# Optimization experiments

Hardware: AMD Instinct MI355X
Metric: run time of the kernel (lower is better)

The kernel has to match this reference:

```python
import jax, jax.numpy as jnp
import numpy as np

B, L, NC, D = 4, 2048, 4096, 128
ITERS = 4
NHEAD = 8
T = L // 2
C2 = 2 * D


def _ln(x, g, b, eps=1e-5):
    m = jnp.mean(x, axis=-1, keepdims=True)
    v = jnp.var(x, axis=-1, keepdims=True)
    return (x - m) * jax.lax.rsqrt(v + eps) * g + b


def _mlp3(x, W1, b1, W2, b2, W3, b3):
    h = jax.nn.relu(x @ W1 + b1)
    h = jax.nn.relu(h @ W2 + b2)
    return h @ W3 + b3


def _lstm(inp, h, c, Wih, Whh, gi, bi, gh, bh, gc, bc):
    gates = _ln(inp @ Wih, gi, bi) + _ln(h @ Whh, gh, bh)
    i, f, g, o = jnp.split(gates, 4, axis=-1)
    cy = _ln(jax.nn.sigmoid(f) * c + jax.nn.sigmoid(i) * jnp.tanh(g), gc, bc)
    hy = jax.nn.sigmoid(o) * jnp.tanh(cy)
    return hy, cy


def _flip(x):
    # flip matrix with full literal counts == permutation swapping pos/neg halves
    half = x.shape[1] // 2
    return jnp.concatenate([x[:, half:], x[:, :half]], axis=1)


def setup_inputs():
    key = jax.random.key(0)
    ks = iter(jax.random.split(key, 64))
    def xav(fi, fo):
        s = float(np.sqrt(6.0 / (fi + fo)))
        return jax.random.uniform(next(ks), (fi, fo), jnp.float32, -s, s)
    def rn(*shape):
        return jax.random.normal(next(ks), shape, jnp.float32)
    inp = {}
    inp['adjacency_matrices'] = (jax.random.uniform(next(ks), (B, L, NC)) < 0.03).astype(jnp.float32)
    inp['batch_lit_counts'] = jnp.full((B,), L, dtype=jnp.int32)
    inp['L_init'] = rn(1, D) / np.sqrt(D).astype(np.float32)
    inp['C_init'] = rn(1, D) / np.sqrt(D).astype(np.float32)
    for p in ('LC', 'CL'):
        for i in (1, 2, 3):
            inp[p + '_W' + str(i)] = xav(D, D)
            inp[p + '_b' + str(i)] = jnp.full((D,), 0.01, jnp.float32)
    for p, isz in (('Lu', 2 * D), ('Cu', D)):
        inp[p + '_Wih'] = rn(isz, 4 * D)  # torch uses raw randn for LSTM weights
        inp[p + '_Whh'] = rn(D, 4 * D)
        for ln, n in (('lni', 4 * D), ('lnh', 4 * D), ('lnc', D)):
            inp[p + '_' + ln + '_g'] = jnp.ones((n,), jnp.float32)
            inp[p + '_' + ln + '_b'] = jnp.zeros((n,), jnp.float32)
    for p in ('k', 'q', 'v'):
        inp['att_W' + p] = xav(C2, C2)
        inp['att_b' + p] = jnp.zeros((C2,), jnp.float32)
    for p in ('asn', 'vote'):
        inp[p + '_W1'] = xav(C2, D)
        inp[p + '_b1'] = jnp.full((D,), 0.01, jnp.float32)
        inp[p + '_W2'] = xav(D, 1)
        inp[p + '_b2'] = jnp.full((1,), 0.01, jnp.float32)
    return inp


def reference(adjacency_matrices, batch_lit_counts, L_init, C_init,
              LC_W1, LC_b1, LC_W2, LC_b2, LC_W3, LC_b3,
              CL_W1, CL_b1, CL_W2, CL_b2, CL_W3, CL_b3,
              Lu_Wih, Lu_Whh, Lu_lni_g, Lu_lni_b, Lu_lnh_g, Lu_lnh_b, Lu_lnc_g, Lu_lnc_b,
              Cu_Wih, Cu_Whh, Cu_lni_g, Cu_lni_b, Cu_lnh_g, Cu_lnh_b, Cu_lnc_g, Cu_lnc_b,
              att_Wk, att_bk, att_Wq, att_bq, att_Wv, att_bv,
              asn_W1, asn_b1, asn_W2, asn_b2, vote_W1, vote_b1, vote_W2, vote_b2):
    A = adjacency_matrices
    Bb, Ll, Cc = A.shape
    Lh = jnp.broadcast_to(L_init, (Bb, Ll, D))
    Lc = jnp.zeros_like(Lh)
    Ch = jnp.broadcast_to(C_init, (Bb, Cc, D))
    Cxc = jnp.zeros_like(Ch)
    for _ in range(ITERS):
        # literal -> clause messages (gather via A^T)
        LC = jnp.einsum('blc,bld->bcd', A, _mlp3(Lh, LC_W1, LC_b1, LC_W2, LC_b2, LC_W3, LC_b3))
        Ch, Cxc = _lstm(LC, Ch, Cxc, Cu_Wih, Cu_Whh, Cu_lni_g, Cu_lni_b, Cu_lnh_g, Cu_lnh_b, Cu_lnc_g, Cu_lnc_b)
        # clause -> literal messages (scatter via A)
        CL = jnp.einsum('blc,bcd->bld', A, _mlp3(Ch, CL_W1, CL_b1, CL_W2, CL_b2, CL_W3, CL_b3))
        Lh, Lc = _lstm(jnp.concatenate([CL, _flip(Lh)], axis=-1), Lh, Lc,
                       Lu_Wih, Lu_Whh, Lu_lni_g, Lu_lni_b, Lu_lnh_g, Lu_lnh_b, Lu_lnc_g, Lu_lnc_b)
    # readout [h_l ; h_{~l}], positive literals only
    read = jnp.concatenate([Lh, _flip(Lh)], axis=-1)[:, :T]  # [B,T,2D]
    half = batch_lit_counts // 2
    mask = (jnp.arange(T)[None, :] < half[:, None]).astype(read.dtype)  # [B,T]
    read = read * mask[:, :, None]
    hd = C2 // NHEAD
    def heads(x, W, b):
        return (x @ W + b).reshape(Bb, T, NHEAD, hd).transpose(0, 2, 1, 3)
    k = heads(read, att_Wk, att_bk)
    q = heads(read, att_Wq, att_bq)
    v = heads(read, att_Wv, att_bv)
    att = jnp.einsum('bhtd,bhsd->bhts', q, k) * (1.0 / np.sqrt(hd))
    sq = (mask[:, None, :, None] * mask[:, None, None, :]) > 0  # [B,1,T,T]
    att = jnp.where(sq, att, -jnp.inf)
    att = jax.nn.softmax(att, axis=-1)
    att = jnp.where(jnp.isnan(att), 0.0, att)
    y = jnp.einsum('bhts,bhsd->bhtd', att, v).transpose(0, 2, 1, 3).reshape(Bb, T, C2)
    def head_mlp(x, W1, b1, W2, b2):
        return jax.nn.sigmoid(jax.nn.relu(x @ W1 + b1) @ W2 + b2)[..., 0]
    assignments = head_mlp(y, asn_W1, asn_b1, asn_W2, asn_b2) * mask  # [B,T]
    vote_vals = head_mlp(y, vote_W1, vote_b1, vote_W2, vote_b2)
    votes = jnp.sum(vote_vals * mask, axis=1) / jnp.maximum(jnp.sum(mask, axis=1), 1.0)
    return votes, assignments
```

## Files before the change

kernel.cpp:

```cpp
#include <hip/hip_runtime.h>


#define B_    4
#define L_    2048
#define NC_   4096
#define D_    128
#define ITERS_ 4
#define NH_   8
#define T_    1024
#define C2_   256
#define HD_   32
#define BL_   (B_*L_)
#define BNC_  (B_*NC_)
#define QS_   768

typedef unsigned short u16;
typedef __attribute__((ext_vector_type(8))) short b16x8;
typedef __attribute__((ext_vector_type(4))) float f32x4;

static __device__ __forceinline__ float bf2f(u16 u){
  union{unsigned int i; float f;} x; x.i = ((unsigned int)u) << 16; return x.f;
}
static __device__ __forceinline__ u16 f2bf(float f){
  union{float f; unsigned int i;} x; x.f = f;
// ... 111 lines not shown
  if ((w & 63) == 0) ss[w >> 6] = pc;
  __syncthreads();
  if (w == 0) cnt_l[row] = ss[0] + ss[1];
}

__global__ __launch_bounds__(256) void k_scan(unsigned* __restrict__ cnt,
    unsigned* __restrict__ off, int n){
  __shared__ unsigned ps[257];
  int t = threadIdx.x;
  int seg = n >> 8;
  int base = t*seg;
  unsigned s = 0;
  for (int i = 0; i < seg; i++) s += cnt[base+i];
  ps[t] = s;
  __syncthreads();
  if (t == 0){
    unsigned run = 0;
    for (int i = 0; i < 256; i++){ unsigned x = ps[i]; ps[i] = run; run += x; }
    ps[256] = run;
  }
  __syncthreads();
  unsigned run = ps[t];
  for (int i = 0; i < seg; i++){ off[base+i] = run; run += cnt[base+i]; cnt[base+i] = 0u; }
  if (t == 0) off[n] = ps[256];
}

__global__ __launch_bounds__(128) void k_fill_l(const unsigned* __restrict__ bits,
    const unsigned* __restrict__ off_l, u16* __restrict__ val_l,
    unsigned* __restrict__ cnt_c){
  const int row = blockIdx.x, w = threadIdx.x;
  const int b = row >> 11;
  unsigned m = bits[(size_t)row*128 + w];
  unsigned pc = __popc(m);
  __shared__ unsigned s[128];
  s[w] = pc; __syncthreads();
  #pragma unroll
  for (int o = 1; o < 128; o <<= 1){
    unsigned v = (w >= o) ? s[w-o] : 0u;
    __syncthreads();
    s[w] += v;
    __syncthreads();
  }
  unsigned base = off_l[row] + s[w] - pc;
  unsigned cb = ((unsigned)b << 12) + w*32;
  while (m){
    int j = __ffs(m) - 1; m &= m - 1;
    val_l[base++] = (u16)(w*32 + j);
    atomicAdd(cnt_c + cb + j, 1u);
  }
}

__global__ __launch_bounds__(256) void k_fill_c(const unsigned* __restrict__ bits,
    const unsigned* __restrict__ off_c, unsigned* __restrict__ cur_c,
    u16* __restrict__ val_c){
  int g = blockIdx.x*256 + threadIdx.x;
  unsigned m = bits[g];
  int row = g >> 7, w = g & 127;
  int b = row >> 11, l = row & (L_-1);
  unsigned cb = ((unsigned)b << 12) + w*32;
  while (m){
    int j = __ffs(m) - 1; m &= m - 1;
    unsigned idx = cb + j;
    unsigned pos = atomicAdd(cur_c + idx, 1u);
    val_c[off_c[idx] + pos] = (u16)l;
  }
}

__global__ __launch_bounds__(256) void k_spmm(const unsigned* __restrict__ off,
    const u16* __restrict__ val, const float* __restrict__ M, float* __restrict__ out,
    int sh1, int sh2){
  int row  = blockIdx.x*4 + (threadIdx.x >> 6);
  int lane = threadIdx.x & 63;
  unsigned p0 = off[row], p1 = off[row+1];
  const float2* Mp = (const float2*)M + (((size_t)(row >> sh1) << sh2) * 64) + lane;
  float x = 0.f, y = 0.f;
  for (unsigned p = p0; p < p1; ++p){
    float2 v = Mp[(size_t)val[p] * 64];
    x += v.x; y += v.y;
  }
  float2 r; r.x = x; r.y = y;
  ((float2*)out)[(size_t)row*64 + lane] = r;
}

__global__ __launch_bounds__(256) void k_mlp3m(const float* __restrict__ X,
    const u16* __restrict__ W1h, const u16* __restrict__ W1l,
    const u16* __restrict__ W2h, const u16* __restrict__ W2l,
    const u16* __restrict__ W3h, const u16* __restrict__ W3l,
    const float* __restrict__ b1, const float* __restrict__ b2,
    const float* __restrict__ b3, float* __restrict__ Y)
{
  __shared__ __align__(16) u16 Ah[32*136];
  __shared__ __align__(16) u16 Al[32*136];
  const int tid = threadIdx.x, lane = tid & 63, wv = tid >> 6;
  const int quad = lane >> 4, l15 = lane & 15;
  const int r0 = blockIdx.x * 32;
  {
    int row = tid >> 3, c0 = (tid & 7)*16;
    const float4* src = (const float4*)(X + (size_t)(r0+row)*128 + c0);
    #pragma unroll
    for (int q4 = 0; q4 < 4; q4++){
      float4 v = src[q4]; int k = c0 + q4*4;
      u16 h,l;
      split2(v.x,h,l); Ah[row*136+k]  =h; Al[row*136+k]  =l;
      split2(v.y,h,l); Ah[row*136+k+1]=h; Al[row*136+k+1]=l;
      split2(v.z,h,l); Ah[row*136+k+2]=h; Al[row*136+k+2]=l;
      split2(v.w,h,l); Ah[row*136+k+3]=h; Al[row*136+k+3]=l;
    }
  }
  __syncthreads();
  const u16* Whs[3] = {W1h, W2h, W3h};
  const u16* Wls[3] = {W1l, W2l, W3l};
  const float* bs[3] = {b1, b2, b3};
  #pragma unroll
  for (int layer = 0; layer < 3; layer++){
    f32x4 acc[2][2] = {};
    #pragma unroll
    for (int ks = 0; ks < 4; ks++){
      b16x8 a_h[2], a_l[2];
      #pragma unroll
      for (int mt = 0; mt < 2; mt++){
        int ao = (mt*16 + l15)*136 + ks*32 + quad*8;
        a_h[mt] = *(const b16x8*)(Ah + ao);
        a_l[mt] = *(const b16x8*)(Al + ao);
      }
      #pragma unroll
      for (int ntl = 0; ntl < 2; ntl++){
        int nt = wv*2 + ntl;
        size_t bo = (size_t)((nt*4 + ks)*64 + lane)*8;
        b16x8 bh = *(const b16x8*)(Whs[layer] + bo);
        b16x8 bl = *(const b16x8*)(Wls[layer] + bo);
        #pragma unroll
        for (int mt = 0; mt < 2; mt++){
          acc[mt][ntl] = __builtin_amdgcn_mfma_f32_16x16x32_bf16(a_h[mt], bh, acc[mt][ntl],0,0,0);
          acc[mt][ntl] = __builtin_amdgcn_mfma_f32_16x16x32_bf16(a_h[mt], bl, acc[mt][ntl],0,0,0);
          acc[mt][ntl] = __builtin_amdgcn_mfma_f32_16x16x32_bf16(a_l[mt], bh, acc[mt][ntl],0,0,0);
        }
      }
    }
    if (layer < 2){
      __syncthreads();
      #pragma unroll
      for (int mt = 0; mt < 2; mt++)
        #pragma unroll
        for (int ntl = 0; ntl < 2; ntl++){
          int col = wv*32 + ntl*16 + l15;
          float bb = bs[layer][col];
          #pragma unroll
          for (int r = 0; r < 4; r++){
            int row = mt*16 + quad*4 + r;
            float v = fmaxf(acc[mt][ntl][r] + bb, 0.f);
            u16 h,l; split2(v,h,l);
            Ah[row*136 + col] = h; Al[row*136 + col] = l;
          }
        }
      __syncthreads();
    } else {
      #pragma unroll
      for (int mt = 0; mt < 2; mt++)
        #pragma unroll
        for (int ntl = 0; ntl < 2; ntl++){
          int col = wv*32 + ntl*16 + l15;
          float bb = bs[2][col];
          #pragma unroll
          for (int r = 0; r < 4; r++){
            int row = mt*16 + quad*4 + r;
            Y[(size_t)(r0+row)*128 + col] = acc[mt][ntl][r] + bb;
          }
        }
    }
  }
}

template<int NSEG>
__global__ __launch_bounds__(256) void k_lstm_mfma(
    const float* __restrict__ A0, const float* __restrict__ A1, const float* __restrict__ A2,
    int flip1,
    const u16* __restrict__ W0h, const u16* __restrict__ W0l,
    const u16* __restrict__ W1h, const u16* __restrict__ W1l,
    const u16* __restrict__ W2h, const u16* __restrict__ W2l,
    const float* __restrict__ lni_g, const float* __restrict__ lni_b,
    const float* __restrict__ lnh_g, const float* __restrict__ lnh_b,
    const float* __restrict__ lnc_g, const float* __restrict__ lnc_b,
    const float* __restrict__ c_in, float* __restrict__ c_out,
    float* __restrict__ h_out)
{
  __shared__ __align__(16) float G[32*516];
  __shared__ float red[4][32][4];
  __shared__ float st[32][4];
  u16* Ah = (u16*)G;
  u16* Al = Ah + 32*136;
  const int tid = threadIdx.x, lane = tid & 63, wv = tid >> 6;
  const int quad = lane >> 4, l15 = lane & 15;
  const int r0 = blockIdx.x * 32;

  f32x4 acc1[2][8] = {}, acc2[2][8] = {};

  #pragma unroll
  for (int s = 0; s < NSEG; ++s){
    const float* Ap = (s==0) ? A0 : ((s==1) ? A1 : A2);
    const u16* Wh = (s==0) ? W0h : ((s==1) ? W1h : W2h);
    const u16* Wl = (s==0) ? W0l : ((s==1) ? W1l : W2l);
    const int fm = (s==1) ? flip1 : 0;
    __syncthreads();
    {
      int row = tid >> 3, c0 = (tid & 7)*16;
      int arow = (r0 + row) ^ fm;
      const float4* src = (const float4*)(Ap + (size_t)arow*128 + c0);
      #pragma unroll
      for (int q4 = 0; q4 < 4; q4++){
        float4 v = src[q4]; int k = c0 + q4*4;
        u16 h,l;
        split2(v.x,h,l); Ah[row*136+k]  =h; Al[row*136+k]  =l;
        split2(v.y,h,l); Ah[row*136+k+1]=h; Al[row*136+k+1]=l;
        split2(v.z,h,l); Ah[row*136+k+2]=h; Al[row*136+k+2]=l;
        split2(v.w,h,l); Ah[row*136+k+3]=h; Al[row*136+k+3]=l;
      }
    }
    __syncthreads();
    f32x4 (*accp)[8] = (s == NSEG-1) ? acc2 : acc1;
    #pragma unroll
    for (int ks = 0; ks < 4; ks++){
      b16x8 a_h[2], a_l[2];
      #pragma unroll
      for (int mt = 0; mt < 2; mt++){
        int ao = (mt*16 + l15)*136 + ks*32 + quad*8;
        a_h[mt] = *(const b16x8*)(Ah + ao);
        a_l[mt] = *(const b16x8*)(Al + ao);
      }
      #pragma unroll
      for (int ntl = 0; ntl < 8; ntl++){
        int nt = wv*8 + ntl;
        size_t bo = (size_t)((nt*4 + ks)*64 + lane)*8;
        b16x8 bh = *(const b16x8*)(Wh + bo);
        b16x8 bl = *(const b16x8*)(Wl + bo);
        #pragma unroll
        for (int mt = 0; mt < 2; mt++){
          accp[mt][ntl] = __builtin_amdgcn_mfma_f32_16x16x32_bf16(a_h[mt], bh, accp[mt][ntl],0,0,0);
          accp[mt][ntl] = __builtin_amdgcn_mfma_f32_16x16x32_bf16(a_h[mt], bl, accp[mt][ntl],0,0,0);
          accp[mt][ntl] = __builtin_amdgcn_mfma_f32_16x16x32_bf16(a_l[mt], bh, accp[mt][ntl],0,0,0);
        }
      }
    }
  }

  #pragma unroll
  for (int mt = 0; mt < 2; mt++)
    #pragma unroll
    for (int r = 0; r < 4; r++){
      float s1=0.f, q1=0.f, s2=0.f, q2=0.f;
      #pragma unroll
      for (int ntl = 0; ntl < 8; ntl++){
        float v1 = acc1[mt][ntl][r]; s1 += v1; q1 += v1*v1;
        float v2 = acc2[mt][ntl][r]; s2 += v2; q2 += v2*v2;
      }
      #pragma unroll
      for (int m = 1; m < 16; m <<= 1){
        s1 += __shfl_xor(s1, m); q1 += __shfl_xor(q1, m);
        s2 += __shfl_xor(s2, m); q2 += __shfl_xor(q2, m);
      }
      if (l15 == 0){
        int row = mt*16 + quad*4 + r;
        red[wv][row][0]=s1; red[wv][row][1]=q1; red[wv][row][2]=s2; red[wv][row][3]=q2;
      }
    }
  __syncthreads();
  if (tid < 32){
    int row = tid;
    float s1 = red[0][row][0]+red[1][row][0]+red[2][row][0]+red[3][row][0];
    float q1 = red[0][row][1]+red[1][row][1]+red[2][row][1]+red[3][row][1];
    float s2 = red[0][row][2]+red[1][row][2]+red[2][row][2]+red[3][row][2];
    float q2 = red[0][row][3]+red[1][row][3]+red[2][row][3]+red[3][row][3];
    const float i512 = 1.f/512.f;
    float m1 = s1*i512, v1 = fmaxf(q1*i512 - m1*m1, 0.f);
    float m2 = s2*i512, v2 = fmaxf(q2*i512 - m2*m2, 0.f);
    st[row][0] = m1; st[row][1] = rsqrtf(v1 + 1e-5f);
    st[row][2] = m2; st[row][3] = rsqrtf(v2 + 1e-5f);
  }
  __syncthreads();

  #pragma unroll
  for (int mt = 0; mt < 2; mt++)
    #pragma unroll
    for (int ntl = 0; ntl < 8; ntl++){
      int col = wv*128 + ntl*16 + l15;
      float gi = lni_g[col], bi = lni_b[col];
      float gh = lnh_g[col], bh = lnh_b[col];
      #pragma unroll
      for (int r = 0; r < 4; r++){
        int row = mt*16 + quad*4 + r;
        float v = (acc1[mt][ntl][r] - st[row][0])*st[row][1]*gi + bi
                + (acc2[mt][ntl][r] - st[row][2])*st[row][3]*gh + bh;
        G[row*516 + col] = v;
      }
    }
  __syncthreads();

  float lcg0 = lnc_g[lane], lcb0 = lnc_b[lane];
  float lcg1 = lnc_g[lane+64], lcb1 = lnc_b[lane+64];
  const float i128 = 1.f/128.f;
  #pragma unroll
  for (int i = 0; i < 8; i++){
    int row = wv*8 + i;
    int rg = r0 + row;
    float cp[2], sc = 0.f, qc = 0.f;
    #pragma unroll
    for (int jj = 0; jj < 2; jj++){
      int c = lane + 64*jj;
      float iv = sigm(G[row*516 + c]);
      float fv = sigm(G[row*516 + 128 + c]);
      float gv = tanhf(G[row*516 + 256 + c]);
      cp[jj] = fv * c_in[(size_t)rg*128 + c] + iv*gv;
      sc += cp[jj]; qc += cp[jj]*cp[jj];
    }
    #pragma unroll
    for (int m = 1; m < 64; m <<= 1){ sc += __shfl_xor(sc, m); qc += __shfl_xor(qc, m); }
    float mc = sc*i128, vc = fmaxf(qc*i128 - mc*mc, 0.f), rsc = rsqrtf(vc + 1e-5f);
    #pragma unroll
    for (int jj = 0; jj < 2; jj++){
      int c = lane + 64*jj;
      float cy = (cp[jj]-mc)*rsc*(jj ? lcg1 : lcg0) + (jj ? lcb1 : lcb0);
      c_out[(size_t)rg*128 + c] = cy;
      float ov = sigm(G[row*516 + 384 + c]);
      h_out[(size_t)rg*128 + c] = ov*tanhf(cy);
    }
  }
}

template<int NT, int KK32, int ACT>
__global__ __launch_bounds__(256) void k_gemm_mfma(const float* __restrict__ A,
    const u16* __restrict__ Wh, const u16* __restrict__ Wl,
    const float* __restrict__ bias, float* __restrict__ Y)
{
  const int N = NT*64;
  const int LDA = KK32*32 + 8;
  __shared__ __align__(16) u16 Ah[32*(KK32*32+8)];
  __shared__ __align__(16) u16 Al[32*(KK32*32+8)];
  const int tid = threadIdx.x, lane = tid & 63, wv = tid >> 6;
  const int quad = lane >> 4, l15 = lane & 15;
  const int r0 = blockIdx.x * 32;
  {
    int row = tid >> 3, c0 = (tid & 7)*(KK32*4);
    const float4* src = (const float4*)(A + (size_t)(r0+row)*(KK32*32) + c0);
    #pragma unroll
    for (int q4 = 0; q4 < KK32; q4++){
      float4 v = src[q4]; int k = c0 + q4*4;
      u16 h,l;
      split2(v.x,h,l); Ah[row*LDA+k]  =h; Al[row*LDA+k]  =l;
      split2(v.y,h,l); Ah[row*LDA+k+1]=h; Al[row*LDA+k+1]=l;
      split2(v.z,h,l); Ah[row*LDA+k+2]=h; Al[row*LDA+k+2]=l;
      split2(v.w,h,l); Ah[row*LDA+k+3]=h; Al[row*LDA+k+3]=l;
    }
  }
  __syncthreads();
  f32x4 acc[2][NT] = {};
  #pragma unroll
  for (int ks = 0; ks < KK32; ks++){
    b16x8 a_h[2], a_l[2];
    #pragma unroll
    for (int mt = 0; mt < 2; mt++){
      int ao = (mt*16 + l15)*LDA + ks*32 + quad*8;
      a_h[mt] = *(const b16x8*)(Ah + ao);
      a_l[mt] = *(const b16x8*)(Al + ao);
    }
    #pragma unroll
    for (int ntl = 0; ntl < NT; ntl++){
      int nt = wv*NT + ntl;
      size_t bo = (size_t)((nt*KK32 + ks)*64 + lane)*8;
      b16x8 bh = *(const b16x8*)(Wh + bo);
      b16x8 bl = *(const b16x8*)(Wl + bo);
      #pragma unroll
      for (int mt = 0; mt < 2; mt++){
        acc[mt][ntl] = __builtin_amdgcn_mfma_f32_16x16x32_bf16(a_h[mt], bh, acc[mt][ntl],0,0,0);
        acc[mt][ntl] = __builtin_amdgcn_mfma_f32_16x16x32_bf16(a_h[mt], bl, acc[mt][ntl],0,0,0);
        acc[mt][ntl] = __builtin_amdgcn_mfma_f32_16x16x32_bf16(a_l[mt], bh, acc[mt][ntl],0,0,0);
      }
    }
  }
  #pragma unroll
  for (int mt = 0; mt < 2; mt++)
    #pragma unroll
    for (int ntl = 0; ntl < NT; ntl++){
      int col = wv*(NT*16) + ntl*16 + l15;
      float bb = bias[col];
      #pragma unroll
      for (int r = 0; r < 4; r++){
        int row = mt*16 + quad*4 + r;
        float v = acc[mt][ntl][r] + bb;
        if (ACT) v = fmaxf(v, 0.f);
        Y[(size_t)(r0+row)*N + col] = v;
      }
    }
}

__global__ __launch_bounds__(256) void k_read(const float* __restrict__ Lh,
    const int* __restrict__ counts, float* __restrict__ rd)
{
  int i = blockIdx.x*256 + threadIdx.x;
  if (i >= B_*T_*D_) return;
  int d = i & (D_-1);
  int r = i >> 7;
  int t = r & (T_-1);
  int b = r >> 10;
  int half = counts[b] / 2; if (half > T_) half = T_;
  float m = (t < half) ? 1.f : 0.f;
  rd[(size_t)r*C2_ + d]      = m * Lh[(size_t)(b*L_ + t)*D_ + d];
  rd[(size_t)r*C2_ + D_ + d] = m * Lh[(size_t)(b*L_ + t + T_)*D_ + d];
}

__global__ __launch_bounds__(256) void k_attn_tile(const float* __restrict__ qkv,
    const int* __restrict__ counts, float* __restrict__ y)
{
  const int b = blockIdx.z, h = blockIdx.y, t0 = blockIdx.x*64;
  int half = counts[b] / 2; if (half > T_) half = T_; if (half < 0) half = 0;
  const int tid = threadIdx.x;
  const int lane = tid & 63, wv = tid >> 6;
  const int lr = tid >> 2, lc = (tid & 3)*8;

  if (t0 >= half){
    float* yp = y + ((size_t)(b*T_ + t0 + lr)*C2_ + h*HD_ + lc);
    #pragma unroll
    for (int j = 0; j < 8; j++) yp[j] = 0.f;
    return;
  }

  __shared__ float Qs[64][36];
  __shared__ float Ks[64][32];
  __shared__ float Ss[64][68];

  {
    const float* qp = qkv + (size_t)(b*T_ + t0 + lr)*QS_ + h*HD_ + lc;
    float4 a0 = *(const float4*)qp;
    float4 a1 = *(const float4*)(qp+4);
    *(float4*)&Qs[lr][lc]   = a0;
    *(float4*)&Qs[lr][lc+4] = a1;
  }

  const int ty = tid >> 4, tx = tid & 15;
  const int sr = wv*16 + (lane & 15);
  const int spart = (lane >> 4) * 16;
  const int rp = lane >> 3, cq = lane & 7;
  const int r0 = wv*16 + rp*2;

  float4 acc0 = {0.f,0.f,0.f,0.f}, acc1 = {0.f,0.f,0.f,0.f};
  float mst = -3e38f, lst = 0.f;
  const float scale = 0.17677669529663687f;
  const int nt = (half + 63) >> 6;

  for (int st = 0; st < nt; ++st){
    const int s0 = st*64;
    __syncthreads();
    {
      const float* kp = qkv + (size_t)(b*T_ + s0 + lr)*QS_ + 256 + h*HD_ + lc;
      float4 k0 = *(const float4*)kp;
      float4 k1 = *(const float4*)(kp+4);
      int key = (lr >> 2) & 7;
      int c0 = lc >> 2;
      *(float4*)&Ks[lr][4*((c0  ) ^ key)] = k0;
      *(float4*)&Ks[lr][4*((c0+1) ^ key)] = k1;
    }
    __syncthreads();

    float s4[4][4];
    #pragma unroll
    for (int i = 0; i < 4; i++)
      #pragma unroll
      for (int j = 0; j < 4; j++) s4[i][j] = 0.f;
    const int xk = tx & 7;
    #pragma unroll
    for (int kk4 = 0; kk4 < 8; kk4++){
      float4 a4[4], b4[4];
      #pragma unroll
      for (int i = 0; i < 4; i++) a4[i] = *(const float4*)&Qs[ty*4+i][kk4*4];
      const int pk = 4*(kk4 ^ xk);
      #pragma unroll
      for (int j = 0; j < 4; j++) b4[j] = *(const float4*)&Ks[tx*4+j][pk];
      #pragma unroll
      for (int i = 0; i < 4; i++)
        #pragma unroll
        for (int j = 0; j < 4; j++)
          s4[i][j] += a4[i].x*b4[j].x + a4[i].y*b4[j].y + a4[i].z*b4[j].z + a4[i].w*b4[j].w;
    }
    #pragma unroll
    for (int i = 0; i < 4; i++){
      float4 w4;
      w4.x = (s0 + tx*4 + 0 < half) ? s4[i][0]*scale : -1e30f;
      w4.y = (s0 + tx*4 + 1 < half) ? s4[i][1]*scale : -1e30f;
      w4.z = (s0 + tx*4 + 2 < half) ? s4[i][2]*scale : -1e30f;
      w4.w = (s0 + tx*4 + 3 < half) ? s4[i][3]*scale : -1e30f;
      *(float4*)&Ss[ty*4+i][tx*4] = w4;
    }

    float pvv[16];
    float vmax = -3e38f;
    #pragma unroll
    for (int c4 = 0; c4 < 4; c4++){
      float4 t4 = *(const float4*)&Ss[sr][spart + c4*4];
      pvv[c4*4+0] = t4.x; pvv[c4*4+1] = t4.y; pvv[c4*4+2] = t4.z; pvv[c4*4+3] = t4.w;
      vmax = fmaxf(vmax, fmaxf(fmaxf(t4.x, t4.y), fmaxf(t4.z, t4.w)));
    }
    vmax = fmaxf(vmax, __shfl_xor(vmax, 16));
    vmax = fmaxf(vmax, __shfl_xor(vmax, 32));
    float nm = fmaxf(mst, vmax);
    float alpha = expf(mst - nm);
    float psum = 0.f;
    #pragma unroll
    for (int c = 0; c < 16; c++){
      float p = expf(pvv[c] - nm);
      pvv[c] = p; psum += p;
    }
    psum += __shfl_xor(psum, 16);
    psum += __shfl_xor(psum, 32);
    lst = lst*alpha + psum;
    mst = nm;
    #pragma unroll
    for (int c4 = 0; c4 < 4; c4++){
      float4 w4; w4.x = pvv[c4*4+0]; w4.y = pvv[c4*4+1]; w4.z = pvv[c4*4+2]; w4.w = pvv[c4*4+3];
      *(float4*)&Ss[sr][spart + c4*4] = w4;
    }
    float al0 = __shfl(alpha, 2*rp);
    float al1 = __shfl(alpha, 2*rp + 1);
    acc0.x *= al0; acc0.y *= al0; acc0.z *= al0; acc0.w *= al0;
    acc1.x *= al1; acc1.y *= al1; acc1.z *= al1; acc1.w *= al1;

    const float* vbase = qkv + (size_t)(b*T_ + s0)*QS_ + 512 + h*HD_ + cq*4;
    #pragma unroll 4
    for (int kk4 = 0; kk4 < 16; kk4++){
      float4 p0 = *(const float4*)&Ss[r0  ][kk4*4];
      float4 p1 = *(const float4*)&Ss[r0+1][kk4*4];
      float4 v0 = *(const float4*)(vbase + (size_t)(kk4*4+0)*QS_);
      float4 v1 = *(const float4*)(vbase + (size_t)(kk4*4+1)*QS_);
      float4 v2 = *(const float4*)(vbase + (size_t)(kk4*4+2)*QS_);
      float4 v3 = *(const float4*)(vbase + (size_t)(kk4*4+3)*QS_);
      acc0.x += p0.x*v0.x + p0.y*v1.x + p0.z*v2.x + p0.w*v3.x;
      acc0.y += p0.x*v0.y + p0.y*v1.y + p0.z*v2.y + p0.w*v3.y;
      acc0.z += p0.x*v0.z + p0.y*v1.z + p0.z*v2.z + p0.w*v3.z;
      acc0.w += p0.x*v0.w + p0.y*v1.w + p0.z*v2.w + p0.w*v3.w;
      acc1.x += p1.x*v0.x + p1.y*v1.x + p1.z*v2.x + p1.w*v3.x;
      acc1.y += p1.x*v0.y + p1.y*v1.y + p1.z*v2.y + p1.w*v3.y;
      acc1.z += p1.x*v0.z + p1.y*v1.z + p1.z*v2.z + p1.w*v3.z;
      acc1.w += p1.x*v0.w + p1.y*v1.w + p1.z*v2.w + p1.w*v3.w;
    }
  }

  float l0 = __shfl(lst, 2*rp);
  float l1 = __shfl(lst, 2*rp + 1);
  float m0 = (t0 + r0     < half && l0 > 0.f) ? 1.f/l0 : 0.f;
  float m1 = (t0 + r0 + 1 < half && l1 > 0.f) ? 1.f/l1 : 0.f;
  float4 o0, o1;
  o0.x = acc0.x*m0; o0.y = acc0.y*m0; o0.z = acc0.z*m0; o0.w = acc0.w*m0;
  o1.x = acc1.x*m1; o1.y = acc1.y*m1; o1.z = acc1.z*m1; o1.w = acc1.w*m1;
  *(float4*)(y + ((size_t)(b*T_ + t0 + r0    )*C2_ + h*HD_ + cq*4)) = o0;
  *(float4*)(y + ((size_t)(b*T_ + t0 + r0 + 1)*C2_ + h*HD_ + cq*4)) = o1;
}

__global__ __launch_bounds__(128) void k_final(const float* __restrict__ hv,
    const float* __restrict__ aW2, const float* __restrict__ ab2,
    const float* __restrict__ vW2, const float* __restrict__ vb2,
    const int* __restrict__ counts, void* __restrict__ outv,
    float* __restrict__ vote_sum, const int* __restrict__ flag)
{
  int row = blockIdx.x, tid = threadIdx.x;
  int b = row / T_, t = row - b*T_;
  int half = counts[b] / 2; if (half > T_) half = T_;
  float pa = hv[(size_t)row*256 + tid]       * aW2[tid];
  float pv = hv[(size_t)row*256 + 128 + tid] * vW2[tid];
  #pragma unroll
  for (int off = 32; off > 0; off >>= 1){ pa += __shfl_down(pa, off); pv += __shfl_down(pv, off); }
  __shared__ float r[2][2];
  int wid = tid >> 6, lane = tid & 63;
  if (lane == 0){ r[0][wid] = pa; r[1][wid] = pv; }
  __syncthreads();
  if (tid == 0){
    float a  = sigm(r[0][0] + r[0][1] + ab2[0]);
    float vv = sigm(r[1][0] + r[1][1] + vb2[0]);
    bool mk = (t < half);
    float av = mk ? a : 0.f;
    if (*flag) ((u16*)outv)[4 + row] = f2bf(av);
    else       ((float*)outv)[4 + row] = av;
    if (mk) atomicAdd(vote_sum + b, vv);
  }
}

__global__ void k_votes(const float* __restrict__ vote_sum, const int* __restrict__ counts,
                        void* __restrict__ outv, const int* __restrict__ flag){
  int b = threadIdx.x;
  if (b < B_){
    int half = counts[b] / 2; if (half > T_) half = T_;
    float den = (float)(half > 1 ? half : 1);
    float vv = vote_sum[b] / den;
    if (*flag) ((u16*)outv)[b] = f2bf(vv);
    else       ((float*)outv)[b] = vv;
  }
}

extern "C" void kernel_launch(void* const* d_in, const int* in_sizes, int n_in,
                              void* d_out, int out_size, void* d_ws, size_t ws_size,
                              hipStream_t stream)
{
  const void* A_adj = d_in[0];
  const int* counts = (const int*)d_in[1];

  const size_t M1 = (size_t)1048576;
  const size_t NEED = (5*M1 + M1 + 2*M1 + 2*M1 + 700416 + 16416 + 8224
                       + 16384 + 8192 + 520000 + 520000 + 32) * sizeof(float);
  if (ws_size < NEED) return;

  float* ws = (float*)d_ws;
  float* R    = ws;
  float* Lc   = R + 5*M1;
  float* Ch   = Lc + M1;
  float* Cc   = Ch + 2*M1;
  float* wp   = Cc + 2*M1;
  unsigned* off_c = (unsigned*)(wp + 700416);
  unsigned* off_l = off_c + 16416;
  unsigned* cnt_c = off_l + 8224;
  unsigned* cnt_l = cnt_c + 16384;
  u16* val_c = (u16*)(cnt_l + 8192);
  u16* val_l = (u16*)((float*)val_c + 520000);
  float* tail = (float*)val_l + 520000;
  float* vote_sum = tail;
  int* flag = (int*)(tail + 8);
  unsigned* bits = (unsigned*)R;

  float* R0 = R, *R1 = R + M1, *R2 = R + 2*M1, *R3 = R + 3*M1, *R4 = R + 4*M1;

  k_detect<<<1, 256, 0, stream>>>((const unsigned int*)A_adj, flag);

  CJobs cj;
  int ncj = 0;
  unsigned off = 0;
  auto cadd = [&](int idx, unsigned n)->float*{
    cj.src[ncj] = d_in[idx]; cj.n[ncj] = n; cj.off[ncj] = off;
    float* p = wp + off; off += (n + 3u) & ~3u; ncj++; return p;
  };
  float* Linit = cadd(2, 128);
  float* Cinit = cadd(3, 128);
  float *LC_b1 = cadd(5, 128), *LC_b2 = cadd(7, 128), *LC_b3 = cadd(9, 128);
  float *CL_b1 = cadd(11,128), *CL_b2 = cadd(13,128), *CL_b3 = cadd(15,128);
  float *Lu_lni_g = cadd(18,512), *Lu_lni_b = cadd(19,512);
  float *Lu_lnh_g = cadd(20,512), *Lu_lnh_b = cadd(21,512);
  float *Lu_lnc_g = cadd(22,128), *Lu_lnc_b = cadd(23,128);
  float *Cu_lni_g = cadd(26,512), *Cu_lni_b = cadd(27,512);
  float *Cu_lnh_g = cadd(28,512), *Cu_lnh_b = cadd(29,512);
  float *Cu_lnc_g = cadd(30,128), *Cu_lnc_b = cadd(31,128);
  float *asn_W2 = cadd(40,128), *asn_b2 = cadd(41,1);
  float *vote_W2 = cadd(44,128), *vote_b2 = cadd(45,1);
  float* bqkv = wp + off;
  cj.src[ncj]=d_in[35]; cj.n[ncj]=256; cj.off[ncj]=off;       ncj++;
  cj.src[ncj]=d_in[33]; cj.n[ncj]=256; cj.off[ncj]=off+256;   ncj++;
  cj.src[ncj]=d_in[37]; cj.n[ncj]=256; cj.off[ncj]=off+512;   ncj++;
  off += 768;
  float* bhv = wp + off;
  cj.src[ncj]=d_in[39]; cj.n[ncj]=128; cj.off[ncj]=off;       ncj++;
  cj.src[ncj]=d_in[43]; cj.n[ncj]=128; cj.off[ncj]=off+128;   ncj++;
  off += 256;
  { dim3 g(2, NCJ_); k_cvt_all<<<g, 256, 0, stream>>>(cj, wp, flag); }

  u16* up = (u16*)(wp + ((off + 3u) & ~3u));
  PJobs pj;
  int npj = 0;
  unsigned uoff = 0;
  auto padd = [&](int idx, unsigned n, unsigned Nw, unsigned koff, unsigned ksb,
                  unsigned dsth, unsigned dstl){
    pj.src[npj]=d_in[idx]; pj.n[npj]=n; pj.N[npj]=Nw; pj.koff[npj]=koff;
    pj.ksb[npj]=ksb; pj.dh[npj]=dsth; pj.dl[npj]=dstl; npj++;
  };
  auto solo = [&](int idx, unsigned n, unsigned Nw, unsigned koff, unsigned ksb,
                  const u16** h, const u16** l){
    padd(idx, n, Nw, koff, ksb, uoff, uoff + n);
    *h = up + uoff; *l = up + uoff + n; uoff += 2*n;
  };
  const u16 *lc1h,*lc1l,*lc2h,*lc2l,*lc3h,*lc3l,*cl1h,*cl1l,*cl2h,*cl2l,*cl3h,*cl3l;
  const u16 *cwih_h,*cwih_l,*cwhh_h,*cwhh_l;
  const u16 *lwa_h,*lwa_l,*lwb_h,*lwb_l,*lwhh_h,*lwhh_l;
  solo(4, 16384,128,0,2,&lc1h,&lc1l);  solo(6, 16384,128,0,2,&lc2h,&lc2l);
  solo(8, 16384,128,0,2,&lc3h,&lc3l);  solo(10,16384,128,0,2,&cl1h,&cl1l);
  solo(12,16384,128,0,2,&cl2h,&cl2l);  solo(14,16384,128,0,2,&cl3h,&cl3l);
  solo(24,65536,512,0,2,&cwih_h,&cwih_l);
  solo(25,65536,512,0,2,&cwhh_h,&cwhh_l);
  solo(16,65536,512,0,  2,&lwa_h,&lwa_l);
  solo(16,65536,512,128,2,&lwb_h,&lwb_l);
  solo(17,65536,512,0,2,&lwhh_h,&lwhh_l);
  const u16* wqkv_h = up + uoff;
  const u16* wqkv_l = up + uoff + 196608;
  padd(34, 65536, 256, 0, 3, uoff,           uoff+196608);
  padd(32, 65536, 256, 0, 3, uoff+65536,     uoff+196608+65536);
  padd(36, 65536, 256, 0, 3, uoff+131072,    uoff+196608+131072);
  uoff += 393216;
  const u16* whv_h = up + uoff;
  const u16* whv_l = up + uoff + 65536;
  padd(38, 32768, 128, 0, 3, uoff,        uoff+65536);
  padd(42, 32768, 128, 0, 3, uoff+32768,  uoff+65536+32768);
  uoff += 131072;
  { dim3 g(256, NPJ_); k_prep<<<g, 256, 0, stream>>>(pj, up, flag); }

  k_zero_u<<<(16384+255)/256, 256, 0, stream>>>(cnt_c, 16384);
  k_pack<<<BL_, 128, 0, stream>>>(A_adj, bits, cnt_l, flag);
  k_scan<<<1, 256, 0, stream>>>(cnt_l, off_l, 8192);
  k_fill_l<<<BL_, 128, 0, stream>>>(bits, off_l, val_l, cnt_c);
  k_scan<<<1, 256, 0, stream>>>(cnt_c, off_c, 16384);
  k_fill_c<<<4096, 256, 0, stream>>>(bits, off_c, cnt_c, val_c);

  k_init<<<(BL_*D_)/256, 256, 0, stream>>>(R0, Lc, Linit, BL_*D_);
  k_init<<<(BNC_*D_)/256, 256, 0, stream>>>(Ch, Cc, Cinit, BNC_*D_);

  for (int it = 0; it < ITERS_; ++it){
    bool ev = ((it & 1) == 0);
    float* cur  = ev ? R0 : R4;
    float* msgL = ev ? R1 : R0;
    float* LCb  = ev ? R2 : R1;
    float* msgC = LCb;
    float* CLb  = ev ? R1 : R3;
    float* nxt  = ev ? R4 : R0;

    k_mlp3m<<<BL_/32, 256, 0, stream>>>(cur, lc1h,lc1l, lc2h,lc2l, lc3h,lc3l,
                                        LC_b1, LC_b2, LC_b3, msgL);
    k_spmm<<<BNC_/4, 256, 0, stream>>>(off_c, val_c, msgL, LCb, 12, 11);
    k_lstm_mfma<2><<<BNC_/32, 256, 0, stream>>>(LCb, Ch, nullptr, 0,
        cwih_h, cwih_l, cwhh_h, cwhh_l, nullptr, nullptr,
        Cu_lni_g, Cu_lni_b, Cu_lnh_g, Cu_lnh_b, Cu_lnc_g, Cu_lnc_b, Cc, Cc, Ch);
    k_mlp3m<<<BNC_/32, 256, 0, stream>>>(Ch, cl1h,cl1l, cl2h,cl2l, cl3h,cl3l,
                                         CL_b1, CL_b2, CL_b3, msgC);
    k_spmm<<<BL_/4, 256, 0, stream>>>(off_l, val_l, msgC, CLb, 11, 12);
    k_lstm_mfma<3><<<BL_/32, 256, 0, stream>>>(CLb, cur, cur, 1024,
        lwa_h, lwa_l, lwb_h, lwb_l, lwhh_h, lwhh_l,
        Lu_lni_g, Lu_lni_b, Lu_lnh_g, Lu_lnh_b, Lu_lnc_g, Lu_lnc_b, Lc, Lc, nxt);
  }
  float* Lh = R0;

  float* readb = Lc;
  float* qkvb  = Ch;
  float* yb    = R1;
  float* hv    = R2;

  k_read<<<(B_*T_*D_)/256, 256, 0, stream>>>(Lh, counts, readb);
  k_gemm_mfma<12,8,0><<<(B_*T_)/32, 256, 0, stream>>>(readb, wqkv_h, wqkv_l, bqkv, qkvb);
  { dim3 g(T_/64, NH_, B_); k_attn_tile<<<g, 256, 0, stream>>>(qkvb, counts, yb); }
  k_gemm_mfma<4,8,1><<<(B_*T_)/32, 256, 0, stream>>>(yb, whv_h, whv_l, bhv, hv);
  k_zero<<<1, 64, 0, stream>>>(vote_sum, B_);
  k_final<<<B_*T_, 128, 0, stream>>>(hv, asn_W2, asn_b2, vote_W2, vote_b2,
                                     counts, d_out, vote_sum, flag);
  k_votes<<<1, 64, 0, stream>>>(vote_sum, counts, d_out, flag);
}
```

Measured before the change: 1.909 ms.

## Widen MFMA kernels to 512 threads, fuse read gather, split attention KV

The MLP, LSTM and dense GEMM kernels now run 8 waves per block, with fewer output tiles per wave, and the GEMMs also split columns over a second grid dimension. The separate read/mask kernel is folded into the QKV GEMM as a masked gather. Attention is split into two key halves computed in parallel, then merged by a new combine kernel using log-sum-exp weights. The aim is more parallelism and less register pressure per wave, at the cost of redundant A-tile staging per column split and an extra kernel launch plus partial-result traffic for attention.

```diff
diff --git a/kernel.cpp b/kernel.cpp
--- a/kernel.cpp
+++ b/kernel.cpp
@@ -217,7 +217,7 @@
   ((float2*)out)[(size_t)row*64 + lane] = r;
 }
 
-__global__ __launch_bounds__(256) void k_mlp3m(const float* __restrict__ X,
+__global__ __launch_bounds__(512) void k_mlp3m(const float* __restrict__ X,
     const u16* __restrict__ W1h, const u16* __restrict__ W1l,
     const u16* __restrict__ W2h, const u16* __restrict__ W2l,
     const u16* __restrict__ W3h, const u16* __restrict__ W3l,
@@ -230,17 +230,18 @@
   const int quad = lane >> 4, l15 = lane & 15;
   const int r0 = blockIdx.x * 32;
   {
-    int row = tid >> 3, c0 = (tid & 7)*16;
+    int row = tid >> 4, c0 = (tid & 15)*8;
     const float4* src = (const float4*)(X + (size_t)(r0+row)*128 + c0);
-    #pragma unroll
-    for (int q4 = 0; q4 < 4; q4++){
-      float4 v = src[q4]; int k = c0 + q4*4;
-      u16 h,l;
-      split2(v.x,h,l); Ah[row*136+k]  =h; Al[row*136+k]  =l;
-      split2(v.y,h,l); Ah[row*136+k+1]=h; Al[row*136+k+1]=l;
-      split2(v.z,h,l); Ah[row*136+k+2]=h; Al[row*136+k+2]=l;
-      split2(v.w,h,l); Ah[row*136+k+3]=h; Al[row*136+k+3]=l;
-    }
+    float4 v0 = src[0], v1 = src[1];
+    u16 h,l;
+    split2(v0.x,h,l); Ah[row*136+c0]  =h; Al[row*136+c0]  =l;
+    split2(v0.y,h,l); Ah[row*136+c0+1]=h; Al[row*136+c0+1]=l;
+    split2(v0.z,h,l); Ah[row*136+c0+2]=h; Al[row*136+c0+2]=l;
+    split2(v0.w,h,l); Ah[row*136+c0+3]=h; Al[row*136+c0+3]=l;
+    split2(v1.x,h,l); Ah[row*136+c0+4]=h; Al[row*136+c0+4]=l;
+    split2(v1.y,h,l); Ah[row*136+c0+5]=h; Al[row*136+c0+5]=l;
+    split2(v1.z,h,l); Ah[row*136+c0+6]=h; Al[row*136+c0+6]=l;
+    split2(v1.w,h,l); Ah[row*136+c0+7]=h; Al[row*136+c0+7]=l;
   }
   __syncthreads();
   const u16* Whs[3] = {W1h, W2h, W3h};
@@ -248,7 +249,7 @@
   const float* bs[3] = {b1, b2, b3};
   #pragma unroll
   for (int layer = 0; layer < 3; layer++){
-    f32x4 acc[2][2] = {};
+    f32x4 acc[2] = {};
     #pragma unroll
     for (int ks = 0; ks < 4; ks++){
       b16x8 a_h[2], a_l[2];
@@ -258,56 +259,45 @@
         a_h[mt] = *(const b16x8*)(Ah + ao);
         a_l[mt] = *(const b16x8*)(Al + ao);
       }
-      #pragma unroll
-      for (int ntl = 0; ntl < 2; ntl++){
-        int nt = wv*2 + ntl;
-        size_t bo = (size_t)((nt*4 + ks)*64 + lane)*8;
-        b16x8 bh = *(const b16x8*)(Whs[layer] + bo);
-        b16x8 bl = *(const b16x8*)(Wls[layer] + bo);
-        #pragma unroll
-        for (int mt = 0; mt < 2; mt++){
-          acc[mt][ntl] = __builtin_amdgcn_mfma_f32_16x16x32_bf16(a_h[mt], bh, acc[mt][ntl],0,0,0);
-          acc[mt][ntl] = __builtin_amdgcn_mfma_f32_16x16x32_bf16(a_h[mt], bl, acc[mt][ntl],0,0,0);
-          acc[mt][ntl] = __builtin_amdgcn_mfma_f32_16x16x32_bf16(a_l[mt], bh, acc[mt][ntl],0,0,0);
-        }
-      }
-    }
+      size_t bo = (size_t)((wv*4 + ks)*64 + lane)*8;
+      b16x8 bh = *(const b16x8*)(Whs[layer] + bo);
+      b16x8 bl = *(const b16x8*)(Wls[layer] + bo);
+      #pragma unroll
+      for (int mt = 0; mt < 2; mt++){
+        acc[mt] = __builtin_amdgcn_mfma_f32_16x16x32_bf16(a_h[mt], bh, acc[mt],0,0,0);
+        acc[mt] = __builtin_amdgcn_mfma_f32_16x16x32_bf16(a_h[mt], bl, acc[mt],0,0,0);
+        acc[mt] = __builtin_amdgcn_mfma_f32_16x16x32_bf16(a_l[mt], bh, acc[mt],0,0,0);
+      }
+    }
+    int col = wv*16 + l15;
     if (layer < 2){
+      float bb = bs[layer][col];
       __syncthreads();
       #pragma unroll
       for (int mt = 0; mt < 2; mt++)
         #pragma unroll
-        for (int ntl = 0; ntl < 2; ntl++){
-          int col = wv*32 + ntl*16 + l15;
-          float bb = bs[layer][col];
-          #pragma unroll
-          for (int r = 0; r < 4; r++){
-            int row = mt*16 + quad*4 + r;
-            float v = fmaxf(acc[mt][ntl][r] + bb, 0.f);
-            u16 h,l; split2(v,h,l);
-            Ah[row*136 + col] = h; Al[row*136 + col] = l;
-          }
+        for (int r = 0; r < 4; r++){
+          int row = mt*16 + quad*4 + r;
+          float v = fmaxf(acc[mt][r] + bb, 0.f);
+          u16 h,l; split2(v,h,l);
+          Ah[row*136 + col] = h; Al[row*136 + col] = l;
         }
       __syncthreads();
     } else {
+      float bb = bs[2][col];
       #pragma unroll
       for (int mt = 0; mt < 2; mt++)
         #pragma unroll
-        for (int ntl = 0; ntl < 2; ntl++){
-          int col = wv*32 + ntl*16 + l15;
-          float bb = bs[2][col];
-          #pragma unroll
-          for (int r = 0; r < 4; r++){
-            int row = mt*16 + quad*4 + r;
-            Y[(size_t)(r0+row)*128 + col] = acc[mt][ntl][r] + bb;
-          }
+        for (int r = 0; r < 4; r++){
+          int row = mt*16 + quad*4 + r;
+          Y[(size_t)(r0+row)*128 + col] = acc[mt][r] + bb;
         }
     }
   }
 }
 
 template<int NSEG>
-__global__ __launch_bounds__(256) void k_lstm_mfma(
+__global__ __launch_bounds__(512) void k_lstm_mfma(
     const float* __restrict__ A0, const float* __restrict__ A1, const float* __restrict__ A2,
     int flip1,
     const u16* __restrict__ W0h, const u16* __restrict__ W0l,
@@ -320,7 +310,7 @@
     float* __restrict__ h_out)
 {
   __shared__ __align__(16) float G[32*516];
-  __shared__ float red[4][32][4];
+  __shared__ float red[8][32][4];
   __shared__ float st[32][4];
   u16* Ah = (u16*)G;
   u16* Al = Ah + 32*136;
@@ -328,7 +318,7 @@
   const int quad = lane >> 4, l15 = lane & 15;
   const int r0 = blockIdx.x * 32;
 
-  f32x4 acc1[2][8] = {}, acc2[2][8] = {};
+  f32x4 acc1[2][4] = {}, acc2[2][4] = {};
 
   #pragma unroll
   for (int s = 0; s < NSEG; ++s){
@@ -338,21 +328,22 @@
     const int fm = (s==1) ? flip1 : 0;
     __syncthreads();
     {
-      int row = tid >> 3, c0 = (tid & 7)*16;
+      int row = tid >> 4, c0 = (tid & 15)*8;
       int arow = (r0 + row) ^ fm;
       const float4* src = (const float4*)(Ap + (size_t)arow*128 + c0);
-      #pragma unroll
-      for (int q4 = 0; q4 < 4; q4++){
-        float4 v = src[q4]; int k = c0 + q4*4;
-        u16 h,l;
-        split2(v.x,h,l); Ah[row*136+k]  =h; Al[row*136+k]  =l;
-        split2(v.y,h,l); Ah[row*136+k+1]=h; Al[row*136+k+1]=l;
-        split2(v.z,h,l); Ah[row*136+k+2]=h; Al[row*136+k+2]=l;
-        split2(v.w,h,l); Ah[row*136+k+3]=h; Al[row*136+k+3]=l;
-      }
+      float4 v0 = src[0], v1 = src[1];
+      u16 h,l;
+      split2(v0.x,h,l); Ah[row*136+c0]  =h; Al[row*136+c0]  =l;
+      split2(v0.y,h,l); Ah[row*136+c0+1]=h; Al[row*136+c0+1]=l;
+      split2(v0.z,h,l); Ah[row*136+c0+2]=h; Al[row*136+c0+2]=l;
+      split2(v0.w,h,l); Ah[row*136+c0+3]=h; Al[row*136+c0+3]=l;
+      split2(v1.x,h,l); Ah[row*136+c0+4]=h; Al[row*136+c0+4]=l;
+      split2(v1.y,h,l); Ah[row*136+c0+5]=h; Al[row*136+c0+5]=l;
+      split2(v1.z,h,l); Ah[row*136+c0+6]=h; Al[row*136+c0+6]=l;
+      split2(v1.w,h,l); Ah[row*136+c0+7]=h; Al[row*136+c0+7]=l;
     }
     __syncthreads();
-    f32x4 (*accp)[8] = (s == NSEG-1) ? acc2 : acc1;
+    f32x4 (*accp)[4] = (s == NSEG-1) ? acc2 : acc1;
     #pragma unroll
     for (int ks = 0; ks < 4; ks++){
       b16x8 a_h[2], a_l[2];
@@ -363,8 +354,8 @@
         a_l[mt] = *(const b16x8*)(Al + ao);
       }
       #pragma unroll
-      for (int ntl = 0; ntl < 8; ntl++){
-        int nt = wv*8 + ntl;
+      for (int ntl = 0; ntl < 4; ntl++){
+        int nt = wv*4 + ntl;
         size_t bo = (size_t)((nt*4 + ks)*64 + lane)*8;
         b16x8 bh = *(const b16x8*)(Wh + bo);
         b16x8 bl = *(const b16x8*)(Wl + bo);
@@ -384,7 +375,7 @@
     for (int r = 0; r < 4; r++){
       float s1=0.f, q1=0.f, s2=0.f, q2=0.f;
       #pragma unroll
-      for (int ntl = 0; ntl < 8; ntl++){
+      for (int ntl = 0; ntl < 4; ntl++){
         float v1 = acc1[mt][ntl][r]; s1 += v1; q1 += v1*v1;
         float v2 = acc2[mt][ntl][r]; s2 += v2; q2 += v2*v2;
       }
@@ -401,10 +392,12 @@
   __syncthreads();
   if (tid < 32){
     int row = tid;
-    float s1 = red[0][row][0]+red[1][row][0]+red[2][row][0]+red[3][row][0];
-    float q1 = red[0][row][1]+red[1][row][1]+red[2][row][1]+red[3][row][1];
-    float s2 = red[0][row][2]+red[1][row][2]+red[2][row][2]+red[3][row][2];
-    float q2 = red[0][row][3]+red[1][row][3]+red[2][row][3]+red[3][row][3];
+    float s1=0.f,q1=0.f,s2=0.f,q2=0.f;
+    #pragma unroll
+    for (int w = 0; w < 8; w++){
+      s1 += red[w][row][0]; q1 += red[w][row][1];
+      s2 += red[w][row][2]; q2 += red[w][row][3];
+    }
     const float i512 = 1.f/512.f;
     float m1 = s1*i512, v1 = fmaxf(q1*i512 - m1*m1, 0.f);
     float m2 = s2*i512, v2 = fmaxf(q2*i512 - m2*m2, 0.f);
@@ -416,8 +409,8 @@
   #pragma unroll
   for (int mt = 0; mt < 2; mt++)
     #pragma unroll
-    for (int ntl = 0; ntl < 8; ntl++){
-      int col = wv*128 + ntl*16 + l15;
+    for (int ntl = 0; ntl < 4; ntl++){
+      int col = wv*64 + ntl*16 + l15;
       float gi = lni_g[col], bi = lni_b[col];
       float gh = lnh_g[col], bh = lnh_b[col];
       #pragma unroll
@@ -434,8 +427,8 @@
   float lcg1 = lnc_g[lane+64], lcb1 = lnc_b[lane+64];
   const float i128 = 1.f/128.f;
   #pragma unroll
-  for (int i = 0; i < 8; i++){
-    int row = wv*8 + i;
+  for (int i = 0; i < 4; i++){
+    int row = wv*4 + i;
     int rg = r0 + row;
     float cp[2], sc = 0.f, qc = 0.f;
     #pragma unroll
@@ -461,29 +454,47 @@
   }
 }
 
-template<int NT, int KK32, int ACT>
-__global__ __launch_bounds__(256) void k_gemm_mfma(const float* __restrict__ A,
+template<int NT, int NSPLIT, int KK32, int ACT, int GATHER>
+__global__ __launch_bounds__(512) void k_gemm_mfma(const float* __restrict__ A,
     const u16* __restrict__ Wh, const u16* __restrict__ Wl,
-    const float* __restrict__ bias, float* __restrict__ Y)
+    const float* __restrict__ bias, float* __restrict__ Y,
+    const int* __restrict__ counts)
 {
-  const int N = NT*64;
+  const int NTOT = NSPLIT*8*NT*16;
   const int LDA = KK32*32 + 8;
   __shared__ __align__(16) u16 Ah[32*(KK32*32+8)];
   __shared__ __align__(16) u16 Al[32*(KK32*32+8)];
   const int tid = threadIdx.x, lane = tid & 63, wv = tid >> 6;
   const int quad = lane >> 4, l15 = lane & 15;
-  const int r0 = blockIdx.x * 32;
+  const int r0 = blockIdx.x * 32, by = blockIdx.y;
   {
-    int row = tid >> 3, c0 = (tid & 7)*(KK32*4);
-    const float4* src = (const float4*)(A + (size_t)(r0+row)*(KK32*32) + c0);
-    #pragma unroll
-    for (int q4 = 0; q4 < KK32; q4++){
-      float4 v = src[q4]; int k = c0 + q4*4;
-      u16 h,l;
-      split2(v.x,h,l); Ah[row*LDA+k]  =h; Al[row*LDA+k]  =l;
-      split2(v.y,h,l); Ah[row*LDA+k+1]=h; Al[row*LDA+k+1]=l;
-      split2(v.z,h,l); Ah[row*LDA+k+2]=h; Al[row*LDA+k+2]=l;
-      split2(v.w,h,l); Ah[row*LDA+k+3]=h; Al[row*LDA+k+3]=l;
+    int row = tid >> 4, c0 = (tid & 15)*(KK32*2);
+    if (GATHER){
+      int r = r0 + row; int b = r >> 10; int t = r & 1023;
+      int half = counts[b] / 2; if (half > T_) half = T_;
+      float msk = (t < half) ? 1.f : 0.f;
+      #pragma unroll
+      for (int q4 = 0; q4 < KK32/2; q4++){
+        int c = c0 + q4*4;
+        const float* src = A + ((size_t)(b*L_ + t + ((c >= 128) ? T_ : 0))*128 + (c & 127));
+        float4 v = *(const float4*)src;
+        u16 h,l;
+        split2(v.x*msk,h,l); Ah[row*LDA+c]  =h; Al[row*LDA+c]  =l;
+        split2(v.y*msk,h,l); Ah[row*LDA+c+1]=h; Al[row*LDA+c+1]=l;
+        split2(v.z*msk,h,l); Ah[row*LDA+c+2]=h; Al[row*LDA+c+2]=l;
+        split2(v.w*msk,h,l); Ah[row*LDA+c+3]=h; Al[row*LDA+c+3]=l;
+      }
+    } else {
+      const float4* src = (const float4*)(A + (size_t)(r0+row)*(KK32*32) + c0);
+      #pragma unroll
+      for (int q4 = 0; q4 < KK32/2; q4++){
+        float4 v = src[q4]; int c = c0 + q4*4;
+        u16 h,l;
+        split2(v.x,h,l); Ah[row*LDA+c]  =h; Al[row*LDA+c]  =l;
+        split2(v.y,h,l); Ah[row*LDA+c+1]=h; Al[row*LDA+c+1]=l;
+        split2(v.z,h,l); Ah[row*LDA+c+2]=h; Al[row*LDA+c+2]=l;
+        split2(v.w,h,l); Ah[row*LDA+c+3]=h; Al[row*LDA+c+3]=l;
+      }
     }
   }
   __syncthreads();
@@ -499,7 +510,7 @@
     }
     #pragma unroll
     for (int ntl = 0; ntl < NT; ntl++){
-      int nt = wv*NT + ntl;
+      int nt = by*(8*NT) + wv*NT + ntl;
       size_t bo = (size_t)((nt*KK32 + ks)*64 + lane)*8;
       b16x8 bh = *(const b16x8*)(Wh + bo);
       b16x8 bl = *(const b16x8*)(Wl + bo);
@@ -515,48 +526,30 @@
   for (int mt = 0; mt < 2; mt++)
     #pragma unroll
     for (int ntl = 0; ntl < NT; ntl++){
-      int col = wv*(NT*16) + ntl*16 + l15;
-      float bb = bias[col];
+      int colg = by*(8*NT*16) + wv*(NT*16) + ntl*16 + l15;
+      float bb = bias[colg];
       #pragma unroll
       for (int r = 0; r < 4; r++){
         int row = mt*16 + quad*4 + r;
         float v = acc[mt][ntl][r] + bb;
         if (ACT) v = fmaxf(v, 0.f);
-        Y[(size_t)(r0+row)*N + col] = v;
-      }
-    }
-}
-
-__global__ __launch_bounds__(256) void k_read(const float* __restrict__ Lh,
-    const int* __restrict__ counts, float* __restrict__ rd)
+        Y[(size_t)(r0+row)*NTOT + colg] = v;
+      }
+    }
+}
+
+__global__ __launch_bounds__(256) void k_attn_split(const float* __restrict__ qkv,
+    const int* __restrict__ counts, float* __restrict__ Pa, float* __restrict__ ML)
 {
-  int i = blockIdx.x*256 + threadIdx.x;
-  if (i >= B_*T_*D_) return;
-  int d = i & (D_-1);
-  int r = i >> 7;
-  int t = r & (T_-1);
-  int b = r >> 10;
-  int half = counts[b] / 2; if (half > T_) half = T_;
-  float m = (t < half) ? 1.f : 0.f;
-  rd[(size_t)r*C2_ + d]      = m * Lh[(size_t)(b*L_ + t)*D_ + d];
-  rd[(size_t)r*C2_ + D_ + d] = m * Lh[(size_t)(b*L_ + t + T_)*D_ + d];
-}
-
-__global__ __launch_bounds__(256) void k_attn_tile(const float* __restrict__ qkv,
-    const int* __restrict__ counts, float* __restrict__ y)
-{
-  const int b = blockIdx.z, h = blockIdx.y, t0 = blockIdx.x*64;
+  const int z = blockIdx.z, b = z >> 1, part = z & 1;
+  const int h = blockIdx.y, t0 = blockIdx.x*64;
   int half = counts[b] / 2; if (half > T_) half = T_; if (half < 0) half = 0;
+  const int sbeg = part*512;
+  const int send = (half < sbeg + 512) ? half : (sbeg + 512);
+  if (t0 >= half || sbeg >= send) return;
   const int tid = threadIdx.x;
   const int lane = tid & 63, wv = tid >> 6;
   const int lr = tid >> 2, lc = (tid & 3)*8;
-
-  if (t0 >= half){
-    float* yp = y + ((size_t)(b*T_ + t0 + lr)*C2_ + h*HD_ + lc);
-    #pragma unroll
-    for (int j = 0; j < 8; j++) yp[j] = 0.f;
-    return;
-  }
 
   __shared__ float Qs[64][36];
   __shared__ float Ks[64][32];
@@ -579,10 +572,10 @@
   float4 acc0 = {0.f,0.f,0.f,0.f}, acc1 = {0.f,0.f,0.f,0.f};
   float mst = -3e38f, lst = 0.f;
   const float scale = 0.17677669529663687f;
-  const int nt = (half + 63) >> 6;
-
-  for (int st = 0; st < nt; ++st){
-    const int s0 = st*64;
+  const int ntile = (send - sbeg + 63) >> 6;
+
+  for (int st = 0; st < ntile; ++st){
+    const int s0 = sbeg + st*64;
     __syncthreads();
     {
       const float* kp = qkv + (size_t)(b*T_ + s0 + lr)*QS_ + 256 + h*HD_ + lc;
@@ -677,15 +670,44 @@
     }
   }
 
-  float l0 = __shfl(lst, 2*rp);
-  float l1 = __shfl(lst, 2*rp + 1);
-  float m0 = (t0 + r0     < half && l0 > 0.f) ? 1.f/l0 : 0.f;
-  float m1 = (t0 + r0 + 1 < half && l1 > 0.f) ? 1.f/l1 : 0.f;
-  float4 o0, o1;
-  o0.x = acc0.x*m0; o0.y = acc0.y*m0; o0.z = acc0.z*m0; o0.w = acc0.w*m0;
-  o1.x = acc1.x*m1; o1.y = acc1.y*m1; o1.z = acc1.z*m1; o1.w = acc1.w*m1;
-  *(float4*)(y + ((size_t)(b*T_ + t0 + r0    )*C2_ + h*HD_ + cq*4)) = o0;
-  *(float4*)(y + ((size_t)(b*T_ + t0 + r0 + 1)*C2_ + h*HD_ + cq*4)) = o1;
+  const int prow0 = (b*NH_ + h)*T_ + t0;
+  float* accP = Pa + (size_t)part*1048576;
+  *(float4*)(accP + (size_t)(prow0 + r0    )*32 + cq*4) = acc0;
+  *(float4*)(accP + (size_t)(prow0 + r0 + 1)*32 + cq*4) = acc1;
+  if (lane < 16){
+    float* mlP = ML + (size_t)part*65536;
+    int rr = prow0 + wv*16 + lane;
+    mlP[(size_t)rr*2]   = mst;
+    mlP[(size_t)rr*2+1] = lst;
+  }
+}
+
+__global__ __launch_bounds__(256) void k_attn_comb(const float* __restrict__ Pa,
+    const float* __restrict__ ML, const int* __restrict__ counts,
+    float* __restrict__ y)
+{
+  int g = blockIdx.x*256 + threadIdx.x;
+  int r = g >> 8, c = g & 255;
+  int b = r >> 10, t = r & 1023;
+  int h = c >> 5, cc = c & 31;
+  int half = counts[b] / 2; if (half > T_) half = T_;
+  float out = 0.f;
+  if (t < half){
+    int prow = (b*NH_ + h)*T_ + t;
+    float m0 = ML[(size_t)prow*2], l0 = ML[(size_t)prow*2+1];
+    float a0 = Pa[(size_t)prow*32 + cc];
+    if (half > 512){
+      float m1 = ML[65536 + (size_t)prow*2], l1 = ML[65536 + (size_t)prow*2+1];
+      float a1 = Pa[1048576 + (size_t)prow*32 + cc];
+      float m = fmaxf(m0, m1);
+      float w0 = expf(m0 - m), w1 = expf(m1 - m);
+      float den = w0*l0 + w1*l1;
+      out = (den > 0.f) ? (w0*a0 + w1*a1)/den : 0.f;
+    } else {
+      out = (l0 > 0.f) ? a0/l0 : 0.f;
+    }
+  }
+  y[(size_t)r*256 + c] = out;
 }
 
 __global__ __launch_bounds__(128) void k_final(const float* __restrict__ hv,
@@ -848,30 +870,32 @@
     float* CLb  = ev ? R1 : R3;
     float* nxt  = ev ? R4 : R0;
 
-    k_mlp3m<<<BL_/32, 256, 0, stream>>>(cur, lc1h,lc1l, lc2h,lc2l, lc3h,lc3l,
+    k_mlp3m<<<BL_/32, 512, 0, stream>>>(cur, lc1h,lc1l, lc2h,lc2l, lc3h,lc3l,
                                         LC_b1, LC_b2, LC_b3, msgL);
     k_spmm<<<BNC_/4, 256, 0, stream>>>(off_c, val_c, msgL, LCb, 12, 11);
-    k_lstm_mfma<2><<<BNC_/32, 256, 0, stream>>>(LCb, Ch, nullptr, 0,
+    k_lstm_mfma<2><<<BNC_/32, 512, 0, stream>>>(LCb, Ch, nullptr, 0,
         cwih_h, cwih_l, cwhh_h, cwhh_l, nullptr, nullptr,
         Cu_lni_g, Cu_lni_b, Cu_lnh_g, Cu_lnh_b, Cu_lnc_g, Cu_lnc_b, Cc, Cc, Ch);
-    k_mlp3m<<<BNC_/32, 256, 0, stream>>>(Ch, cl1h,cl1l, cl2h,cl2l, cl3h,cl3l,
+    k_mlp3m<<<BNC_/32, 512, 0, stream>>>(Ch, cl1h,cl1l, cl2h,cl2l, cl3h,cl3l,
                                          CL_b1, CL_b2, CL_b3, msgC);
     k_spmm<<<BL_/4, 256, 0, stream>>>(off_l, val_l, msgC, CLb, 11, 12);
-    k_lstm_mfma<3><<<BL_/32, 256, 0, stream>>>(CLb, cur, cur, 1024,
+    k_lstm_mfma<3><<<BL_/32, 512, 0, stream>>>(CLb, cur, cur, 1024,
         lwa_h, lwa_l, lwb_h, lwb_l, lwhh_h, lwhh_l,
         Lu_lni_g, Lu_lni_b, Lu_lnh_g, Lu_lnh_b, Lu_lnc_g, Lu_lnc_b, Lc, Lc, nxt);
   }
   float* Lh = R0;
 
-  float* readb = Lc;
   float* qkvb  = Ch;
   float* yb    = R1;
   float* hv    = R2;
 
-  k_read<<<(B_*T_*D_)/256, 256, 0, stream>>>(Lh, counts, readb);
-  k_gemm_mfma<12,8,0><<<(B_*T_)/32, 256, 0, stream>>>(readb, wqkv_h, wqkv_l, bqkv, qkvb);
-  { dim3 g(T_/64, NH_, B_); k_attn_tile<<<g, 256, 0, stream>>>(qkvb, counts, yb); }
-  k_gemm_mfma<4,8,1><<<(B_*T_)/32, 256, 0, stream>>>(yb, whv_h, whv_l, bhv, hv);
+  { dim3 g((B_*T_)/32, 2);
+    k_gemm_mfma<3,2,8,0,1><<<g, 512, 0, stream>>>(Lh, wqkv_h, wqkv_l, bqkv, qkvb, counts); }
+  { dim3 g(T_/64, NH_, B_*2);
+    k_attn_split<<<g, 256, 0, stream>>>(qkvb, counts, R3, Lc); }
+  k_attn_comb<<<4096, 256, 0, stream>>>(R3, Lc, counts, yb);
+  { dim3 g((B_*T_)/32, 2);
+    k_gemm_mfma<1,2,8,1,0><<<g, 512, 0, stream>>>(yb, whv_h, whv_l, bhv, hv, counts); }
   k_zero<<<1, 64, 0, stream>>>(vote_sum, B_);
   k_final<<<B_*T_, 128, 0, stream>>>(hv, asn_W2, asn_b2, vote_W2, vote_b2,
                                      counts, d_out, vote_sum, flag);
```

After: 1.692 ms. 11.3% less time.
